# Kernel optimization log

Hardware: AMD Instinct MI355X
Metric: run time of the kernel (lower is better)

Reference implementation:

```python
import jax, jax.numpy as jnp
import numpy as np

EPS = 1e-5


def _conv(x, w, groups=1):
    # x: NCHW, w: OIHW, stride 1, padding k//2 == SAME for k=3
    return jax.lax.conv_general_dilated(
        x, w, window_strides=(1, 1), padding='SAME',
        feature_group_count=groups,
        dimension_numbers=('NCHW', 'OIHW', 'NCHW'))


def _bn(x, gamma, beta, mean, var):
    # eval-mode BatchNorm2d
    s = gamma * jax.lax.rsqrt(var + EPS)
    return x * s[None, :, None, None] + (beta - mean * s)[None, :, None, None]


def _bilinear_up_kernel(ch, k):
    # dla_up.fill_up_weights: bilinear upsampling kernel, shape (ch, 1, k, k)
    f = (k + 1) // 2
    c = (2 * f - 1 - f % 2) / (2.0 * f)
    i = np.arange(k)
    w1d = 1.0 - np.abs(i / f - c)
    w2d = np.outer(w1d, w1d).astype(np.float32)  # (k, k)
    return jnp.asarray(np.broadcast_to(w2d, (ch, 1, k, k)).copy())


def setup_inputs() -> dict:
    key = jax.random.key(0)
    ks = jax.random.split(key, 8)
    B, C, H, W = 16, 32, 128, 128
    OUT, NL = 8, 4
    layers = jax.random.normal(ks[0], (NL + 1, B, C, H, W), jnp.float32)
    node_w = jax.random.normal(ks[1], (NL, C, 2 * C, 3, 3), jnp.float32) * 0.05
    node_gamma = jnp.ones((NL, C), jnp.float32)
    node_beta = jnp.zeros((NL, C), jnp.float32)
    node_mean = jax.random.normal(ks[2], (NL, C), jnp.float32) * 0.1
    node_var = jax.random.uniform(ks[3], (NL, C), jnp.float32, 0.5, 1.5)
    final_w = jax.random.normal(ks[4], (OUT, C, 3, 3), jnp.float32) * 0.05
    final_gamma = jnp.ones((OUT,), jnp.float32)
    final_beta = jnp.zeros((OUT,), jnp.float32)
    final_mean = jax.random.normal(ks[5], (OUT,), jnp.float32) * 0.1
    final_var = jax.random.uniform(ks[6], (OUT,), jnp.float32, 0.5, 1.5)
    up_w = _bilinear_up_kernel(OUT, 4)  # frozen depthwise transpose-conv weight
    return dict(layers=layers, node_w=node_w, node_gamma=node_gamma,
                node_beta=node_beta, node_mean=node_mean, node_var=node_var,
                final_w=final_w, final_gamma=final_gamma, final_beta=final_beta,
                final_mean=final_mean, final_var=final_var, up_w=up_w)


def reference(layers, node_w, node_gamma, node_beta, node_mean, node_var,
              final_w, final_gamma, final_beta, final_mean, final_var, up_w):
    x = layers[0]
    n_layers = node_w.shape[0]
    for i in range(n_layers):  # fixed small structural loop
        h = jnp.concatenate([x, layers[i + 1]], axis=1)  # [B, 2C, H, W]
        x = jax.nn.relu(_bn(_conv(h, node_w[i]),
                            node_gamma[i], node_beta[i], node_mean[i], node_var[i]))
    x = jnp.tanh(_bn(_conv(x, final_w),
                     final_gamma, final_beta, final_mean, final_var))
    # depthwise ConvTranspose2d(k=4, stride=2, pad=1): equivalent fractionally
    # strided conv with flipped kernel, lhs_dilation=2, padding k-1-pad=2
    groups = up_w.shape[0]
    x = jax.lax.conv_general_dilated(
        x, up_w[:, :, ::-1, ::-1], window_strides=(1, 1),
        padding=[(2, 2), (2, 2)], lhs_dilation=(2, 2),
        feature_group_count=groups,
        dimension_numbers=('NCHW', 'OIHW', 'NCHW'))  # [B, OUT, 2H, 2W]
    # vectorized form of the per-row / per-col delta loops
    Ho, Wo = x.shape[2], x.shape[3]
    row_ramp = jnp.arange(Ho, dtype=x.dtype) / Ho  # delta_i = i / H
    col_ramp = jnp.arange(Wo, dtype=x.dtype) / Wo  # delta_j = j / W
    x = x.at[:, 0].add(row_ramp[None, :, None])
    x = x.at[:, 1].add(col_ramp[None, None, :])
    return x
```

## Files before the change

kernel.cpp:

```cpp
#include <hip/hip_runtime.h>
#include <hip/hip_bf16.h>
#include <cmath>

using bf16 = __hip_bfloat16;
typedef _Float16 f16x8 __attribute__((ext_vector_type(8)));
typedef float f32x16 __attribute__((ext_vector_type(16)));

__device__ __forceinline__ float ldin(const void* p, size_t i, int f) {
    return f ? ((const float*)p)[i] : __bfloat162float(((const bf16*)p)[i]);
}

__device__ __forceinline__ float bfu(unsigned short u) {
    union { unsigned u32; float f; } x; x.u32 = (unsigned)u << 16; return x.f;
}

__global__ void detect_kernel(const unsigned short* __restrict__ u, int* __restrict__ flag) {
    __shared__ int s_bad;
    if (threadIdx.x == 0) s_bad = 0;
    __syncthreads();
    int base = blockIdx.x * 256 + threadIdx.x;
    int bad = 0;
#pragma unroll
    for (int k = 0; k < 4; ++k) {
        unsigned short v = u[2 * (base + k * 16384)];
        int e = (v >> 7) & 0xFF;
        if (e == 0xFF || (e == 0 && (v & 0x7FFF))) bad++;
    }
    if (bad) atomicAdd(&s_bad, bad);
    __syncthreads();
    if (threadIdx.x == 0 && s_bad) atomicAdd(&flag[1], s_bad);
}

__global__ void pack_kernel(const void* __restrict__ nw, const void* __restrict__ ng,
                            const void* __restrict__ nb, const void* __restrict__ nm,
                            const void* __restrict__ nv, const void* __restrict__ fw,
                            const void* __restrict__ fg, const void* __restrict__ fb,
                            const void* __restrict__ fm, const void* __restrict__ fv,
                            const void* __restrict__ upw, const int* __restrict__ flag,
                            char* __restrict__ ws) {
    const int f = flag[1] > 32;
    int i = blockIdx.x * 256 + threadIdx.x;
    _Float16* wpkN = (_Float16*)(ws + 160);
    _Float16* wpkF = (_Float16*)(ws + 147616);
    float* upwf  = (float*)(ws + 166048);
    float* nbias = (float*)(ws + 166560);
    float* fbias = (float*)(ws + 167072);
    if (i < 73728) {
        int e = i & 7, lane = (i >> 3) & 63, rest = i >> 9;
        int t = rest % 9, rest2 = rest / 9;
        int kc = rest2 & 3, lay = rest2 >> 2;
        int oc = lane & 31, ic = kc * 16 + ((lane >> 5) << 3) + e;
        float s = ldin(ng, lay * 32 + oc, f) * rsqrtf(ldin(nv, lay * 32 + oc, f) + 1e-5f);
        float w = ldin(nw, ((size_t)(lay * 32 + oc) * 64 + ic) * 9 + t, f);
        wpkN[i] = (_Float16)(w * s);
    } else if (i < 82944) {
        int j = i - 73728;
        int e = j & 7, lane = (j >> 3) & 63, rest = j >> 9;
        int t = rest % 9, kc = rest / 9;
        int oc = lane & 31, ic = kc * 16 + ((lane >> 5) << 3) + e;
        float v = 0.f;
        if (oc < 8) {
            float s = ldin(fg, oc, f) * rsqrtf(ldin(fv, oc, f) + 1e-5f);
            v = ldin(fw, ((size_t)(oc * 32 + ic)) * 9 + t, f) * s;
        }
        wpkF[j] = (_Float16)v;
    } else if (i < 83072) {
        int k = i - 82944;
        upwf[k] = ldin(upw, k, f);
    } else if (i < 83200) {
        int k = i - 83072;
        float s = ldin(ng, k, f) * rsqrtf(ldin(nv, k, f) + 1e-5f);
        nbias[k] = ldin(nb, k, f) - ldin(nm, k, f) * s;
    } else if (i < 83232) {
        int k = i - 83200;
        float v = 0.f;
        if (k < 8) {
            float s = ldin(fg, k, f) * rsqrtf(ldin(fv, k, f) + 1e-5f);
            v = ldin(fb, k, f) - ldin(fm, k, f) * s;
        }
        fbias[k] = v;
    }
}

__device__ __forceinline__ void stage_nchw_vec(char* lds, const void* src,
                                               size_t base_elem, int f, int tid,
                                               int x0g, int y0g) {
    for (int job = tid; job < 1280; job += 256) {
        int i = job & 7, t = job >> 3;
        int row = t % 10, c2 = t / 10;
        int gy = y0g - 1 + row;
        float a0[4] = {0.f, 0.f, 0.f, 0.f}, a1[4] = {0.f, 0.f, 0.f, 0.f};
        if (gy >= 0 && gy < 128) {
            size_t e0 = base_elem + (size_t)(c2 * 2) * 16384 + (size_t)gy * 128 + x0g + i * 4;
            if (f) {
                float4 v0 = *(const float4*)((const float*)src + e0);
                float4 v1 = *(const float4*)((const float*)src + e0 + 16384);
                a0[0] = v0.x; a0[1] = v0.y; a0[2] = v0.z; a0[3] = v0.w;
                a1[0] = v1.x; a1[1] = v1.y; a1[2] = v1.z; a1[3] = v1.w;
            } else {
                ushort4 v0 = *(const ushort4*)((const unsigned short*)src + e0);
                ushort4 v1 = *(const ushort4*)((const unsigned short*)src + e0 + 16384);
                a0[0] = bfu(v0.x); a0[1] = bfu(v0.y); a0[2] = bfu(v0.z); a0[3] = bfu(v0.w);
                a1[0] = bfu(v1.x); a1[1] = bfu(v1.y); a1[2] = bfu(v1.z); a1[3] = bfu(v1.w);
            }
        }
#pragma unroll
        for (int j = 0; j < 4; ++j) {
            int x = 1 + i * 4 + j;
            union { _Float16 h[2]; unsigned u; } pk;
            pk.h[0] = (_Float16)a0[j]; pk.h[1] = (_Float16)a1[j];
            *(unsigned*)(lds + row * 2176 + (x << 6) + ((c2 << 2) ^ ((x & 3) << 4))) = pk.u;
        }
    }
    for (int job = tid; job < 320; job += 256) {
        int e = job & 1, t = job >> 1;
        int row = t % 10, c2 = t / 10;
        int gy = y0g - 1 + row;
        int x = e ? 33 : 0;
        int gx = x0g - 1 + x;
        float v0 = 0.f, v1 = 0.f;
        if (gy >= 0 && gy < 128 && gx >= 0 && gx < 128) {
            size_t e0 = base_elem + (size_t)(c2 * 2) * 16384 + (size_t)gy * 128 + gx;
            v0 = ldin(src, e0, f);
            v1 = ldin(src, e0 + 16384, f);
        }
        union { _Float16 h[2]; unsigned u; } pk;
        pk.h[0] = (_Float16)v0; pk.h[1] = (_Float16)v1;
        *(unsigned*)(lds + row * 2176 + (x << 6) + ((c2 << 2) ^ ((x & 3) << 4))) = pk.u;
    }
}

__device__ __forceinline__ void stage_nhwc(char* lds, const _Float16* xh, int tid,
                                           int b, int x0g, int y0g) {
    for (int q = tid; q < 1360; q += 256) {
        int p = q >> 2, j = q & 3;
        int iyy = p / 34, x = p - iyy * 34;
        int c0 = (j ^ (x & 3)) << 3;
        int gy = y0g - 1 + iyy, gx = x0g - 1 + x;
        uint4 v = {0u, 0u, 0u, 0u};
        if (gy >= 0 && gy < 128 && gx >= 0 && gx < 128)
            v = *(const uint4*)(xh + (((size_t)(b * 128 + gy) * 128 + gx) * 32 + c0));
        *(uint4*)(lds + (q << 4)) = v;
    }
}

__device__ __forceinline__ void conv_plane(const char* lds, const _Float16* wseg,
                                           int lane, int wid, int lh,
                                           f32x16& acc0, f32x16& acc1) {
    const int l31 = lane & 31;
#pragma unroll
    for (int kc = 0; kc < 2; ++kc) {
        f16x8 bfr[9];
#pragma unroll
        for (int t = 0; t < 9; ++t)
            bfr[t] = *(const f16x8*)(wseg + (size_t)((kc * 9 + t) * 64 + lane) * 8);
        const int cbase = (kc << 5) + (lh << 4);
#pragma unroll
        for (int iy = 0; iy < 4; ++iy) {
            const int rowoff = ((wid << 1) + iy) * 2176;
#pragma unroll
            for (int kx = 0; kx < 3; ++kx) {
                const int x = l31 + kx;
                const f16x8 a = *(const f16x8*)(lds + rowoff + (x << 6)
                                                + (cbase ^ ((x & 3) << 4)));
#pragma unroll
                for (int ky = 0; ky < 3; ++ky) {
                    const int y = iy - ky;
                    if (y == 0)
                        acc0 = __builtin_amdgcn_mfma_f32_32x32x16_f16(a, bfr[ky * 3 + kx], acc0, 0, 0, 0);
                    else if (y == 1)
                        acc1 = __builtin_amdgcn_mfma_f32_32x32x16_f16(a, bfr[ky * 3 + kx], acc1, 0, 0, 0);
                }
            }
        }
    }
}

__global__ __launch_bounds__(256, 4) void node_conv_mfma(
    const void* __restrict__ xprev, int xprev_nchw, int xprev_slice,
    const void* __restrict__ layers, int skip_slice,
    const _Float16* __restrict__ wl, const float* __restrict__ bias,
    const int* __restrict__ flag, _Float16* __restrict__ out) {
    __shared__ char lds[21760];
    const int f = flag[1] > 32;
    const int tid = threadIdx.x;
    const int x0g = blockIdx.x << 5, y0g = blockIdx.y << 3, b = blockIdx.z;
    const int lane = tid & 63, wid = tid >> 6;
    const int l31 = lane & 31, lh = lane >> 5;

    f32x16 acc0, acc1;
#pragma unroll
    for (int r = 0; r < 16; ++r) { acc0[r] = 0.f; acc1[r] = 0.f; }

    if (xprev_nchw)
        stage_nchw_vec(lds, xprev, (size_t)xprev_slice * 8388608 + (size_t)b * 524288,
                       f, tid, x0g, y0g);
    else
        stage_nhwc(lds, (const _Float16*)xprev, tid, b, x0g, y0g);
    __syncthreads();
    conv_plane(lds, wl, lane, wid, lh, acc0, acc1);
    __syncthreads();

    stage_nchw_vec(lds, layers, (size_t)skip_slice * 8388608 + (size_t)b * 524288,
                   f, tid, x0g, y0g);
    __syncthreads();
    conv_plane(lds, wl + 9216, lane, wid, lh, acc0, acc1);

    const float bs = bias[l31];
#pragma unroll
    for (int y = 0; y < 2; ++y) {
        const int gy = y0g + (wid << 1) + y;
        const f32x16 av = y ? acc1 : acc0;
#pragma unroll
        for (int r = 0; r < 16; ++r) {
            const int xr = (r & 3) + ((r >> 2) << 3) + (lh << 2);
            const float v = fmaxf(av[r] + bs, 0.f);
            out[((size_t)(b * 128 + gy) * 128 + (x0g + xr)) * 32 + l31] = (_Float16)v;
        }
    }
}

__global__ __launch_bounds__(256, 4) void final_conv_mfma(
    const _Float16* __restrict__ xin, const _Float16* __restrict__ wf,
    const float* __restrict__ fbias, _Float16* __restrict__ outF) {
    __shared__ char lds[21760];
    const int tid = threadIdx.x;
    const int x0g = blockIdx.x << 5, y0g = blockIdx.y << 3, b = blockIdx.z;
    const int lane = tid & 63, wid = tid >> 6;
    const int l31 = lane & 31, lh = lane >> 5;

    stage_nhwc(lds, xin, tid, b, x0g, y0g);
    __syncthreads();

    f32x16 acc0, acc1;
#pragma unroll
    for (int r = 0; r < 16; ++r) { acc0[r] = 0.f; acc1[r] = 0.f; }
    conv_plane(lds, wf, lane, wid, lh, acc0, acc1);

    const float bs = fbias[l31];
#pragma unroll
    for (int y = 0; y < 2; ++y) {
        const int gy = y0g + (wid << 1) + y;
        const f32x16 av = y ? acc1 : acc0;
#pragma unroll
        for (int r = 0; r < 16; ++r) {
            const int xr = (r & 3) + ((r >> 2) << 3) + (lh << 2);
            const float v = tanhf(av[r] + bs);
            if (l31 < 8)
                outF[((size_t)(b * 128 + gy) * 128 + (x0g + xr)) * 8 + l31] = (_Float16)v;
        }
    }
}

__global__ __launch_bounds__(256) void upsample_q(
    const _Float16* __restrict__ F, const float* __restrict__ wf,
    const int* __restrict__ flag, void* __restrict__ out) {
    const int f = flag[1] > 32;
    int i = blockIdx.x * 256 + threadIdx.x;
    int qx = i & 127, qy = (i >> 7) & 127, b = i >> 14;

    f16x8 inb[3][3];
#pragma unroll
    for (int jy = 0; jy < 3; ++jy)
#pragma unroll
        for (int jx = 0; jx < 3; ++jx) {
            int iy = qy - 1 + jy, ix = qx - 1 + jx;
            f16x8 v;
#pragma unroll
            for (int c = 0; c < 8; ++c) v[c] = (_Float16)0.f;
            if (iy >= 0 && iy < 128 && ix >= 0 && ix < 128)
                v = *(const f16x8*)(F + (((size_t)(b * 128 + iy) * 128 + ix) << 3));
            inb[jy][jx] = v;
        }

    float acc[32];
#pragma unroll
    for (int k = 0; k < 32; ++k) acc[k] = 0.f;
#pragma unroll
    for (int ky = 0; ky < 4; ++ky) {
        const int dy = 1 - (ky & 1), jy = 2 - ((ky + 1) >> 1);
#pragma unroll
        for (int kx = 0; kx < 4; ++kx) {
            const int dx = 1 - (kx & 1), jx = 2 - ((kx + 1) >> 1);
            const f16x8 p = inb[jy][jx];
#pragma unroll
            for (int c = 0; c < 8; ++c)
                acc[c * 4 + dy * 2 + dx] =
                    fmaf((float)p[c], wf[c * 16 + ky * 4 + kx], acc[c * 4 + dy * 2 + dx]);
        }
    }
#pragma unroll
    for (int d = 0; d < 4; ++d) {
        acc[d]     += (float)(2 * qy + (d >> 1)) * (1.0f / 256.0f);
        acc[4 + d] += (float)(2 * qx + (d & 1)) * (1.0f / 256.0f);
    }
#pragma unroll
    for (int c = 0; c < 8; ++c)
#pragma unroll
        for (int dy2 = 0; dy2 < 2; ++dy2) {
            size_t a = ((size_t)(b * 8 + c) * 256 + (qy * 2 + dy2)) * 256 + qx * 2;
            float v0 = acc[c * 4 + dy2 * 2], v1 = acc[c * 4 + dy2 * 2 + 1];
            if (f) {
                *(float2*)((float*)out + a) = make_float2(v0, v1);
            } else {
                union { bf16 h; unsigned short u; } u0, u1;
                u0.h = __float2bfloat16(v0); u1.h = __float2bfloat16(v1);
                ((unsigned*)out)[a >> 1] = (unsigned)u0.u | ((unsigned)u1.u << 16);
            }
        }
}

extern "C" void kernel_launch(void* const* d_in, const int* in_sizes, int n_in,
                              void* d_out, int out_size, void* d_ws, size_t ws_size,
                              hipStream_t stream) {
    const void* layers = d_in[0];
    const void* node_w = d_in[1];
    const void* ng     = d_in[2];
    const void* nb     = d_in[3];
    const void* nm     = d_in[4];
    const void* nv     = d_in[5];
    const void* fw     = d_in[6];
    const void* fg     = d_in[7];
    const void* fb     = d_in[8];
    const void* fm     = d_in[9];
    const void* fv     = d_in[10];
    const void* upw    = d_in[11];

    char* ws = (char*)d_ws;
    int* dflag       = (int*)d_ws;
    _Float16* wpkN   = (_Float16*)(ws + 160);
    _Float16* wpkF   = (_Float16*)(ws + 147616);
    float* upwf      = (float*)(ws + 166048);
    float* nbias     = (float*)(ws + 166560);
    float* fbias     = (float*)(ws + 167072);
    _Float16* X      = (_Float16*)(ws + 167424);
    _Float16* Y      = (_Float16*)d_out;

    hipMemsetAsync(dflag, 0, 16, stream);
    detect_kernel<<<64, 256, 0, stream>>>((const unsigned short*)layers, dflag);
    pack_kernel<<<326, 256, 0, stream>>>(node_w, ng, nb, nm, nv,
                                         fw, fg, fb, fm, fv, upw, dflag, ws);

    dim3 g(4, 16, 16), blk(256);
    node_conv_mfma<<<g, blk, 0, stream>>>(layers, 1, 0, layers, 1,
                                          wpkN, nbias, dflag, X);
    node_conv_mfma<<<g, blk, 0, stream>>>(X, 0, 0, layers, 2,
                                          wpkN + 18432, nbias + 32, dflag, Y);
    node_conv_mfma<<<g, blk, 0, stream>>>(Y, 0, 0, layers, 3,
                                          wpkN + 2 * 18432, nbias + 64, dflag, X);
    node_conv_mfma<<<g, blk, 0, stream>>>(X, 0, 0, layers, 4,
                                          wpkN + 3 * 18432, nbias + 96, dflag, Y);
    final_conv_mfma<<<g, blk, 0, stream>>>(Y, wpkF, fbias, X);
    upsample_q<<<1024, 256, 0, stream>>>(X, upwf, dflag, d_out);
}
```

Before: 456.8 us.

## Restage NCHW tiles per pixel with rotation swizzle, fast tanh, relax occupancy

Replaces the NCHW staging routine so each thread gathers 8 channels for one pixel and writes a full 16-byte chunk to LDS. The XOR swizzle becomes a rotation swizzle, applied consistently in the NHWC staging and the MFMA operand reads. Halo columns are now handled in the same loop instead of a separate pass. Also swaps tanhf for an exp-based fast tanh, unrolls the epilogue stores explicitly, and lowers launch_bounds min-blocks from 4 to 3. The per-pixel gather uses 8 scalar strided global loads in place of vector loads, which may hurt coalescing.

```diff
diff --git a/kernel.cpp b/kernel.cpp
--- a/kernel.cpp
+++ b/kernel.cpp
@@ -13,6 +13,8 @@
 __device__ __forceinline__ float bfu(unsigned short u) {
     union { unsigned u32; float f; } x; x.u32 = (unsigned)u << 16; return x.f;
 }
+
+__device__ __forceinline__ int swq(int X) { return (X + (X >> 2)) & 3; }
 
 __global__ void detect_kernel(const unsigned short* __restrict__ u, int* __restrict__ flag) {
     __shared__ int s_bad;
@@ -82,64 +84,43 @@
     }
 }
 
-__device__ __forceinline__ void stage_nchw_vec(char* lds, const void* src,
-                                               size_t base_elem, int f, int tid,
-                                               int x0g, int y0g) {
-    for (int job = tid; job < 1280; job += 256) {
-        int i = job & 7, t = job >> 3;
-        int row = t % 10, c2 = t / 10;
-        int gy = y0g - 1 + row;
-        float a0[4] = {0.f, 0.f, 0.f, 0.f}, a1[4] = {0.f, 0.f, 0.f, 0.f};
-        if (gy >= 0 && gy < 128) {
-            size_t e0 = base_elem + (size_t)(c2 * 2) * 16384 + (size_t)gy * 128 + x0g + i * 4;
+__device__ __forceinline__ void stage_nchw_g(char* lds, const void* src,
+                                             size_t base_elem, int f, int tid,
+                                             int x0g, int y0g) {
+    for (int job = tid; job < 1360; job += 256) {
+        int c = job / 340, rest = job - c * 340;
+        int row = rest / 34, X = rest - row * 34;
+        int gy = y0g - 1 + row, gx = x0g - 1 + X;
+        union { _Float16 h[8]; uint4 v; } pk;
+        if (gy >= 0 && gy < 128 && gx >= 0 && gx < 128) {
+            size_t e0 = base_elem + (size_t)(c * 8) * 16384 + (size_t)gy * 128 + gx;
             if (f) {
-                float4 v0 = *(const float4*)((const float*)src + e0);
-                float4 v1 = *(const float4*)((const float*)src + e0 + 16384);
-                a0[0] = v0.x; a0[1] = v0.y; a0[2] = v0.z; a0[3] = v0.w;
-                a1[0] = v1.x; a1[1] = v1.y; a1[2] = v1.z; a1[3] = v1.w;
+#pragma unroll
+                for (int j = 0; j < 8; ++j)
+                    pk.h[j] = (_Float16)(((const float*)src)[e0 + (size_t)j * 16384]);
             } else {
-                ushort4 v0 = *(const ushort4*)((const unsigned short*)src + e0);
-                ushort4 v1 = *(const ushort4*)((const unsigned short*)src + e0 + 16384);
-                a0[0] = bfu(v0.x); a0[1] = bfu(v0.y); a0[2] = bfu(v0.z); a0[3] = bfu(v0.w);
-                a1[0] = bfu(v1.x); a1[1] = bfu(v1.y); a1[2] = bfu(v1.z); a1[3] = bfu(v1.w);
+#pragma unroll
+                for (int j = 0; j < 8; ++j)
+                    pk.h[j] = (_Float16)bfu(((const unsigned short*)src)[e0 + (size_t)j * 16384]);
             }
-        }
-#pragma unroll
-        for (int j = 0; j < 4; ++j) {
-            int x = 1 + i * 4 + j;
-            union { _Float16 h[2]; unsigned u; } pk;
-            pk.h[0] = (_Float16)a0[j]; pk.h[1] = (_Float16)a1[j];
-            *(unsigned*)(lds + row * 2176 + (x << 6) + ((c2 << 2) ^ ((x & 3) << 4))) = pk.u;
-        }
-    }
-    for (int job = tid; job < 320; job += 256) {
-        int e = job & 1, t = job >> 1;
-        int row = t % 10, c2 = t / 10;
-        int gy = y0g - 1 + row;
-        int x = e ? 33 : 0;
-        int gx = x0g - 1 + x;
-        float v0 = 0.f, v1 = 0.f;
-        if (gy >= 0 && gy < 128 && gx >= 0 && gx < 128) {
-            size_t e0 = base_elem + (size_t)(c2 * 2) * 16384 + (size_t)gy * 128 + gx;
-            v0 = ldin(src, e0, f);
-            v1 = ldin(src, e0 + 16384, f);
-        }
-        union { _Float16 h[2]; unsigned u; } pk;
-        pk.h[0] = (_Float16)v0; pk.h[1] = (_Float16)v1;
-        *(unsigned*)(lds + row * 2176 + (x << 6) + ((c2 << 2) ^ ((x & 3) << 4))) = pk.u;
+        } else {
+            pk.v = make_uint4(0u, 0u, 0u, 0u);
+        }
+        int slot = (c + swq(X)) & 3;
+        *(uint4*)(lds + row * 2176 + (X << 6) + (slot << 4)) = pk.v;
     }
 }
 
 __device__ __forceinline__ void stage_nhwc(char* lds, const _Float16* xh, int tid,
                                            int b, int x0g, int y0g) {
     for (int q = tid; q < 1360; q += 256) {
-        int p = q >> 2, j = q & 3;
-        int iyy = p / 34, x = p - iyy * 34;
-        int c0 = (j ^ (x & 3)) << 3;
-        int gy = y0g - 1 + iyy, gx = x0g - 1 + x;
+        int p = q >> 2, s = q & 3;
+        int row = p / 34, X = p - row * 34;
+        int c = (s - swq(X)) & 3;
+        int gy = y0g - 1 + row, gx = x0g - 1 + X;
         uint4 v = {0u, 0u, 0u, 0u};
         if (gy >= 0 && gy < 128 && gx >= 0 && gx < 128)
-            v = *(const uint4*)(xh + (((size_t)(b * 128 + gy) * 128 + gx) * 32 + c0));
+            v = *(const uint4*)(xh + (((size_t)(b * 128 + gy) * 128 + gx) * 32 + c * 8));
         *(uint4*)(lds + (q << 4)) = v;
     }
 }
@@ -154,15 +135,15 @@
 #pragma unroll
         for (int t = 0; t < 9; ++t)
             bfr[t] = *(const f16x8*)(wseg + (size_t)((kc * 9 + t) * 64 + lane) * 8);
-        const int cbase = (kc << 5) + (lh << 4);
+        const int chunk = (kc << 1) | lh;
 #pragma unroll
         for (int iy = 0; iy < 4; ++iy) {
             const int rowoff = ((wid << 1) + iy) * 2176;
 #pragma unroll
             for (int kx = 0; kx < 3; ++kx) {
-                const int x = l31 + kx;
-                const f16x8 a = *(const f16x8*)(lds + rowoff + (x << 6)
-                                                + (cbase ^ ((x & 3) << 4)));
+                const int X = l31 + kx;
+                const int slot = (chunk + swq(X)) & 3;
+                const f16x8 a = *(const f16x8*)(lds + rowoff + (X << 6) + (slot << 4));
 #pragma unroll
                 for (int ky = 0; ky < 3; ++ky) {
                     const int y = iy - ky;
@@ -176,7 +157,7 @@
     }
 }
 
-__global__ __launch_bounds__(256, 4) void node_conv_mfma(
+__global__ __launch_bounds__(256, 3) void node_conv_mfma(
     const void* __restrict__ xprev, int xprev_nchw, int xprev_slice,
     const void* __restrict__ layers, int skip_slice,
     const _Float16* __restrict__ wl, const float* __restrict__ bias,
@@ -193,34 +174,43 @@
     for (int r = 0; r < 16; ++r) { acc0[r] = 0.f; acc1[r] = 0.f; }
 
     if (xprev_nchw)
-        stage_nchw_vec(lds, xprev, (size_t)xprev_slice * 8388608 + (size_t)b * 524288,
-                       f, tid, x0g, y0g);
+        stage_nchw_g(lds, xprev, (size_t)xprev_slice * 8388608 + (size_t)b * 524288,
+                     f, tid, x0g, y0g);
     else
         stage_nhwc(lds, (const _Float16*)xprev, tid, b, x0g, y0g);
     __syncthreads();
     conv_plane(lds, wl, lane, wid, lh, acc0, acc1);
     __syncthreads();
 
-    stage_nchw_vec(lds, layers, (size_t)skip_slice * 8388608 + (size_t)b * 524288,
-                   f, tid, x0g, y0g);
+    stage_nchw_g(lds, layers, (size_t)skip_slice * 8388608 + (size_t)b * 524288,
+                 f, tid, x0g, y0g);
     __syncthreads();
     conv_plane(lds, wl + 9216, lane, wid, lh, acc0, acc1);
 
     const float bs = bias[l31];
-#pragma unroll
-    for (int y = 0; y < 2; ++y) {
-        const int gy = y0g + (wid << 1) + y;
-        const f32x16 av = y ? acc1 : acc0;
+    {
+        const int gy = y0g + (wid << 1);
 #pragma unroll
         for (int r = 0; r < 16; ++r) {
             const int xr = (r & 3) + ((r >> 2) << 3) + (lh << 2);
-            const float v = fmaxf(av[r] + bs, 0.f);
-            out[((size_t)(b * 128 + gy) * 128 + (x0g + xr)) * 32 + l31] = (_Float16)v;
-        }
-    }
-}
-
-__global__ __launch_bounds__(256, 4) void final_conv_mfma(
+            out[((size_t)(b * 128 + gy) * 128 + (x0g + xr)) * 32 + l31] =
+                (_Float16)fmaxf(acc0[r] + bs, 0.f);
+        }
+#pragma unroll
+        for (int r = 0; r < 16; ++r) {
+            const int xr = (r & 3) + ((r >> 2) << 3) + (lh << 2);
+            out[((size_t)(b * 128 + gy + 1) * 128 + (x0g + xr)) * 32 + l31] =
+                (_Float16)fmaxf(acc1[r] + bs, 0.f);
+        }
+    }
+}
+
+__device__ __forceinline__ float ftanh(float x) {
+    float e = __expf(2.f * x);
+    return 1.f - 2.f / (e + 1.f);
+}
+
+__global__ __launch_bounds__(256, 3) void final_conv_mfma(
     const _Float16* __restrict__ xin, const _Float16* __restrict__ wf,
     const float* __restrict__ fbias, _Float16* __restrict__ outF) {
     __shared__ char lds[21760];
@@ -238,16 +228,19 @@
     conv_plane(lds, wf, lane, wid, lh, acc0, acc1);
 
     const float bs = fbias[l31];
-#pragma unroll
-    for (int y = 0; y < 2; ++y) {
-        const int gy = y0g + (wid << 1) + y;
-        const f32x16 av = y ? acc1 : acc0;
+    if (l31 < 8) {
+        const int gy = y0g + (wid << 1);
 #pragma unroll
         for (int r = 0; r < 16; ++r) {
             const int xr = (r & 3) + ((r >> 2) << 3) + (lh << 2);
-            const float v = tanhf(av[r] + bs);
-            if (l31 < 8)
-                outF[((size_t)(b * 128 + gy) * 128 + (x0g + xr)) * 8 + l31] = (_Float16)v;
+            outF[((size_t)(b * 128 + gy) * 128 + (x0g + xr)) * 8 + l31] =
+                (_Float16)ftanh(acc0[r] + bs);
+        }
+#pragma unroll
+        for (int r = 0; r < 16; ++r) {
+            const int xr = (r & 3) + ((r >> 2) << 3) + (lh << 2);
+            outF[((size_t)(b * 128 + gy + 1) * 128 + (x0g + xr)) * 8 + l31] =
+                (_Float16)ftanh(acc1[r] + bs);
         }
     }
 }
```

After: 482.0 us. +5.5%, slower.
